# Performance work log

Hardware: AMD Instinct MI355X
Metric: run time of the kernel (lower is better)

## Reference

```python
import jax, jax.numpy as jnp
import numpy as np

B, T, N, D = 4, 8, 256, 1024
DH, KD, VD, IM, KC, H, L = 768, 576, 1152, 2048, 4, 12, 5
DK, DV = KD // H, VD // H

def _rms(x, w, eps=1e-6):
    return x * jax.lax.rsqrt(jnp.mean(x * x, -1, keepdims=True) + eps) * w

def _l2(x, eps=1e-6):
    return x * jax.lax.rsqrt(jnp.sum(x * x, -1, keepdims=True) + eps)

def _conv_silu(x, w):
    # depthwise causal conv1d over tokens: x [b,n,C], w [C,K]
    K = w.shape[1]
    xp = jnp.pad(x, ((0, 0), (K - 1, 0), (0, 0)))
    y = sum(xp[:, j:j + x.shape[1], :] * w[:, j] for j in range(K))
    return jax.nn.silu(y)

def _gdn_attn(x, p):
    b, n, _ = x.shape
    q = _l2(_conv_silu(x @ p['wq'].T, p['cq']).reshape(b, n, H, DK))
    k = _l2(_conv_silu(x @ p['wk'].T, p['ck']).reshape(b, n, H, DK))
    v = _conv_silu(x @ p['wv'].T, p['cv']).reshape(b, n, H, DV)
    beta = jax.nn.sigmoid(x @ p['wb'].T)                                   # [b,n,H]
    g = -jnp.exp(p['A_log']) * jax.nn.softplus(x @ p['wa'].T + p['dt_bias'])  # mamba-style log-decay
    scale = DK ** -0.5

    def step(S, inp):
        qt, kt, vt, gt, bt = inp
        S = S * jnp.exp(gt)[..., None, None]                               # [b,H,dk,dv] gated decay
        v_old = jnp.einsum('bhk,bhkv->bhv', kt, S)
        dv = bt[..., None] * (vt - v_old)                                  # delta rule update
        S = S + kt[..., None] * dv[:, :, None, :]
        o = jnp.einsum('bhk,bhkv->bhv', qt, S)
        return S, o

    xs = (jnp.moveaxis(q * scale, 1, 0), jnp.moveaxis(k, 1, 0), jnp.moveaxis(v, 1, 0),
          jnp.moveaxis(g, 1, 0), jnp.moveaxis(beta, 1, 0))
    S0 = jnp.zeros((b, H, DK, DV), x.dtype)
    _, o = jax.lax.scan(step, S0, xs)
    o = jnp.moveaxis(o, 0, 1)                                              # [b,n,H,dv]
    gate = (x @ p['wg'].T).reshape(b, n, H, DV)
    o = _rms(o, p['onorm']) * gate * jax.nn.sigmoid(gate)                  # RMSNorm + swish gate
    return o.reshape(b, n, VD) @ p['wo'].T

def _block(x, p):
    x = x + _gdn_attn(_rms(x, p['n1']), p)
    h = _rms(x, p['n2'])
    return x + (jax.nn.silu(h @ p['w1'].T) * (h @ p['w3'].T)) @ p['w2'].T

def _forward(z, actions, enc_w, enc_b, ap_w, ap_b, temb, ln_w, ln_b, dec_w, dec_b, lp, block_fn):
    zt = z.reshape(B, T, N, D)
    feat = zt @ enc_w.T + enc_b                                            # 1x1 conv == per-token linear
    act = jnp.broadcast_to(actions[:, :, None, :], (B, T, N, actions.shape[-1]))
    tok = jnp.concatenate([feat, act], -1) @ ap_w.T + ap_b
    tpos = jnp.minimum(jnp.arange(T), temb.shape[0] - 1)
    tok = tok + temb[tpos][None, :, None, :]
    x = tok.reshape(B * T, N, DH)                                          # timesteps independent -> fold into batch
    for i in range(L):
        p = {k: v[i] for k, v in lp.items()}
        x = block_fn(x, p)
    mu = jnp.mean(x, -1, keepdims=True)
    var = jnp.mean((x - mu) ** 2, -1, keepdims=True)
    x = (x - mu) * jax.lax.rsqrt(var + 1e-5) * ln_w + ln_b                 # final LayerNorm
    delta = x @ dec_w.T + dec_b
    return (zt + delta.reshape(B, T, N, D)).reshape(B, T * N, D)

def setup_inputs():
    key = jax.random.key(0)
    cnt = [0]
    def nrm(shape, s=0.02):
        cnt[0] += 1
        return jax.random.normal(jax.random.fold_in(key, cnt[0]), shape, jnp.float32) * s
    A = 2
    return dict(
        z=nrm((B, T * N, D), 1.0), actions=nrm((B, T, A), 1.0),
        enc_w=nrm((DH, D)), enc_b=jnp.zeros((DH,), jnp.float32),
        ap_w=nrm((DH, DH + A)), ap_b=jnp.zeros((DH,), jnp.float32),
        temb=nrm((T + 1, DH)),
        ln_w=jnp.ones((DH,), jnp.float32), ln_b=jnp.zeros((DH,), jnp.float32),
        dec_w=nrm((D, DH)), dec_b=jnp.zeros((D,), jnp.float32),
        n1=jnp.ones((L, DH), jnp.float32), n2=jnp.ones((L, DH), jnp.float32),
        wq=nrm((L, KD, DH)), cq=nrm((L, KD, KC), 0.3),
        wk=nrm((L, KD, DH)), ck=nrm((L, KD, KC), 0.3),
        wv=nrm((L, VD, DH)), cv=nrm((L, VD, KC), 0.3),
        wb=nrm((L, H, DH)), wa=nrm((L, H, DH)),
        A_log=jnp.log(jax.random.uniform(jax.random.fold_in(key, 777), (L, H), jnp.float32, 1.0, 16.0)),
        dt_bias=nrm((L, H), 0.1),
        wg=nrm((L, VD, DH)), onorm=jnp.ones((L, DV), jnp.float32),
        wo=nrm((L, DH, VD)),
        w1=nrm((L, IM, DH)), w2=nrm((L, DH, IM)), w3=nrm((L, IM, DH)),
    )

def reference(z, actions, enc_w, enc_b, ap_w, ap_b, temb, ln_w, ln_b, dec_w, dec_b,
              n1, n2, wq, cq, wk, ck, wv, cv, wb, wa, A_log, dt_bias, wg, onorm, wo, w1, w2, w3):
    lp = dict(n1=n1, n2=n2, wq=wq, cq=cq, wk=wk, ck=ck, wv=wv, cv=cv, wb=wb, wa=wa,
              A_log=A_log, dt_bias=dt_bias, wg=wg, onorm=onorm, wo=wo, w1=w1, w2=w2, w3=w3)
    return _forward(z, actions, enc_w, enc_b, ap_w, ap_b, temb, ln_w, ln_b, dec_w, dec_b, lp, _block)
```

## Files before the change

### kernel.cpp

```cpp
#include <hip/hip_runtime.h>
#include <math.h>

#define RTOT 8192
#define SEQL 256
#define DHC 768
#define KDC 576
#define VDC 1152
#define IMC 2048
#define NHC 12
#define DKC 48
#define DVC 96
#define NLAY 5

typedef float f4 __attribute__((ext_vector_type(4)));
typedef __bf16 v8bf __attribute__((ext_vector_type(8)));

__device__ __forceinline__ float sigmoidf_(float x){ return 1.0f/(1.0f+expf(-x)); }
__device__ __forceinline__ float siluf_(float x){ return x/(1.0f+expf(-x)); }

__device__ __forceinline__ void gl16(const void* g, void* l) {
    __builtin_amdgcn_global_load_lds((const __attribute__((address_space(1))) void*)g,
                                     (__attribute__((address_space(3))) void*)l, 16, 0, 0);
}
#define MFMA_BF16(a,b,c) __builtin_amdgcn_mfma_f32_16x16x32_bf16((a),(b),(c),0,0,0)

template<bool HASAL>
__global__ __launch_bounds__(256)
void gemm3_kernel(const __bf16* __restrict__ Ah, const __bf16* __restrict__ Al,
                  const __bf16* __restrict__ Wh, const __bf16* __restrict__ Wl,
                  int K, int ldc, int mode,
                  float* Cf, const float* bias, const float* bias2, const float* res,
                  __bf16* Ch, __bf16* Cl, const float* aux)
{
    __shared__ __bf16 sAh[128*32], sBh[128*32], sBl[128*32];
    __shared__ __bf16 sAl[HASAL ? 128*32 : 16];
    const int tid  = threadIdx.x;
    const int m0   = blockIdx.y * 128, n0 = blockIdx.x * 128;
    const int lane = tid & 63, wv = tid >> 6;
    const int wm   = (wv & 1) * 64, wn = (wv >> 1) * 64;

    const int o0 = tid * 16, o1 = o0 + 4096;
    const int r0 = o0 >> 6, s0 = (o0 >> 4) & 3;
    const int r1 = o1 >> 6, s1 = (o1 >> 4) & 3;
    const int k0 = (s0 ^ ((r0 >> 1) & 3)) * 8;
    const int k1 = (s1 ^ ((r1 >> 1) & 3)) * 8;

    const __bf16* gA0h = Ah + (size_t)(m0 + r0) * K + k0;
    const __bf16* gA1h = Ah + (size_t)(m0 + r1) * K + k1;
    const __bf16* gA0l = HASAL ? (Al + (size_t)(m0 + r0) * K + k0) : nullptr;
    const __bf16* gA1l = HASAL ? (Al + (size_t)(m0 + r1) * K + k1) : nullptr;
    const __bf16* gB0h = Wh + (size_t)(n0 + r0) * K + k0;
    const __bf16* gB1h = Wh + (size_t)(n0 + r1) * K + k1;
    const __bf16* gB0l = Wl + (size_t)(n0 + r0) * K + k0;
    const __bf16* gB1l = Wl + (size_t)(n0 + r1) * K + k1;

    const int fr = lane & 15, g8 = lane >> 4;
    int aoff[4], boff[4];
    #pragma unroll
    for (int f = 0; f < 4; ++f) {
        int ra = wm + f*16 + fr;
        aoff[f] = ra*32 + (g8 ^ ((ra >> 1) & 3)) * 8;
        int rb = wn + f*16 + fr;
        boff[f] = rb*32 + (g8 ^ ((rb >> 1) & 3)) * 8;
    }

    f4 acc[4][4];
    const f4 zero4 = {0.f, 0.f, 0.f, 0.f};
    #pragma unroll
    for (int i = 0; i < 4; ++i)
        #pragma unroll
        for (int j = 0; j < 4; ++j) acc[i][j] = zero4;

    for (int kt = 0; kt < K; kt += 32) {
        gl16(gA0h + kt, (char*)sAh + o0);
        gl16(gA1h + kt, (char*)sAh + o1);
        if constexpr (HASAL) {
            gl16(gA0l + kt, (char*)sAl + o0);
            gl16(gA1l + kt, (char*)sAl + o1);
        }
        gl16(gB0h + kt, (char*)sBh + o0);
        gl16(gB1h + kt, (char*)sBh + o1);
        gl16(gB0l + kt, (char*)sBl + o0);
        gl16(gB1l + kt, (char*)sBl + o1);
        __syncthreads();

        v8bf bhv[4], blv[4];
        #pragma unroll
        for (int f = 0; f < 4; ++f) {
            bhv[f] = *(const v8bf*)(sBh + boff[f]);
            blv[f] = *(const v8bf*)(sBl + boff[f]);
        }
        #pragma unroll
        for (int i = 0; i < 4; ++i) {
            v8bf ahv = *(const v8bf*)(sAh + aoff[i]);
            v8bf alv;
            if constexpr (HASAL) alv = *(const v8bf*)(sAl + aoff[i]);
            #pragma unroll
            for (int j = 0; j < 4; ++j) {
                f4 t = acc[i][j];
                if constexpr (HASAL) t = MFMA_BF16(alv, bhv[j], t);
                t = MFMA_BF16(ahv, blv[j], t);
                acc[i][j] = MFMA_BF16(ahv, bhv[j], t);
            }
        }
        __syncthreads();
    }

    const int rb4 = (lane >> 4) * 4;
    #pragma unroll
    for (int i = 0; i < 4; ++i) {
        #pragma unroll
        for (int jf = 0; jf < 4; ++jf) {
            int col = n0 + wn + jf*16 + fr;
            #pragma unroll
            for (int j = 0; j < 4; ++j) {
                int row = m0 + wm + i*16 + rb4 + j;
                size_t idx = (size_t)row * ldc + col;
                float v = acc[i][jf][j];
                if (bias)  v += bias[col];
                if (bias2) v += bias2[(size_t)(row >> 8) * ldc + col];
                if (res)   v += res[idx];
                if (mode == 2) v = siluf_(aux[idx]) * v;
                if (mode == 0) {
                    Cf[idx] = v;
                } else {
                    __bf16 h = (__bf16)v;
                    Ch[idx] = h;
                    if (Cl) Cl[idx] = (__bf16)(v - (float)h);
                }
            }
        }
    }
}

struct CvtBatch8 {
    const float* src[8];
    __bf16* dh[8];
    __bf16* dl[8];
    int ldv[8];
    int cols[8];
    int rowend[8];
};

__global__ __launch_bounds__(256)
void cvt_batch_kernel(CvtBatch8 b, int njobs)
{
    int r = blockIdx.x;
    int j = 0;
    while (j < njobs - 1 && r >= b.rowend[j]) ++j;
    int row0 = (j == 0) ? 0 : b.rowend[j-1];
    int lr = r - row0;
    const float* s = b.src[j] + (size_t)lr * b.ldv[j];
    __bf16* ph = b.dh[j] + (size_t)lr * b.cols[j];
    __bf16* pl = b.dl[j] + (size_t)lr * b.cols[j];
    int cols = b.cols[j];
    for (int c = threadIdx.x; c < cols; c += 256) {
        float v = s[c];
        __bf16 hh = (__bf16)v;
        ph[c] = hh;
        pl[c] = (__bf16)(v - (float)hh);
    }
}

__global__ __launch_bounds__(256)
void bias2_kernel(const float* __restrict__ actions, const float* __restrict__ ap_w,
                  const float* __restrict__ ap_b, const float* __restrict__ temb,
                  float* __restrict__ B2)
{
    int bt = blockIdx.x;
    int t  = bt & 7;
    float a0 = actions[bt*2], a1 = actions[bt*2+1];
    for (int c = threadIdx.x; c < DHC; c += 256)
        B2[bt*DHC + c] = ap_b[c] + temb[t*DHC + c] + a0*ap_w[c*770 + 768] + a1*ap_w[c*770 + 769];
}

__global__ __launch_bounds__(256)
void rmsnorm_kernel(const float* __restrict__ X, const float* __restrict__ w,
                    __bf16* __restrict__ Yh, __bf16* __restrict__ Yl)
{
    int row = blockIdx.x, tid = threadIdx.x;
    const float* xr = X + (size_t)row*DHC;
    float v0 = xr[tid], v1 = xr[tid+256], v2 = xr[tid+512];
    __shared__ float red[256];
    red[tid] = v0*v0 + v1*v1 + v2*v2;
    __syncthreads();
    for (int s = 128; s; s >>= 1) { if (tid < s) red[tid] += red[tid+s]; __syncthreads(); }
    float r = 1.0f/sqrtf(red[0]/768.0f + 1e-6f);
    float y0 = v0*r*w[tid], y1 = v1*r*w[tid+256], y2 = v2*r*w[tid+512];
    __bf16* ph = Yh + (size_t)row*DHC;
    __bf16* pl = Yl + (size_t)row*DHC;
    __bf16 h0 = (__bf16)y0, h1 = (__bf16)y1, h2 = (__bf16)y2;
    ph[tid] = h0;     pl[tid]     = (__bf16)(y0 - (float)h0);
    ph[tid+256] = h1; pl[tid+256] = (__bf16)(y1 - (float)h1);
    ph[tid+512] = h2; pl[tid+512] = (__bf16)(y2 - (float)h2);
}

__global__ __launch_bounds__(256)
void layernorm_kernel(const float* __restrict__ X, const float* __restrict__ w,
                      const float* __restrict__ b, __bf16* __restrict__ Yh,
                      __bf16* __restrict__ Yl)
{
    int row = blockIdx.x, tid = threadIdx.x;
    const float* xr = X + (size_t)row*DHC;
    float v0 = xr[tid], v1 = xr[tid+256], v2 = xr[tid+512];
    __shared__ float rs[256], rs2[256];
    rs[tid]  = v0+v1+v2;
    rs2[tid] = v0*v0+v1*v1+v2*v2;
    __syncthreads();
    for (int s = 128; s; s >>= 1) { if (tid < s) { rs[tid]+=rs[tid+s]; rs2[tid]+=rs2[tid+s]; } __syncthreads(); }
    float mu  = rs[0]/768.0f;
    float var = rs2[0]/768.0f - mu*mu;
    float r = 1.0f/sqrtf(var + 1e-5f);
    float y0 = (v0-mu)*r*w[tid]     + b[tid];
    float y1 = (v1-mu)*r*w[tid+256] + b[tid+256];
    float y2 = (v2-mu)*r*w[tid+512] + b[tid+512];
    __bf16* ph = Yh + (size_t)row*DHC;
    __bf16* pl = Yl + (size_t)row*DHC;
    __bf16 h0 = (__bf16)y0, h1 = (__bf16)y1, h2 = (__bf16)y2;
    ph[tid] = h0;     pl[tid]     = (__bf16)(y0 - (float)h0);
    ph[tid+256] = h1; pl[tid+256] = (__bf16)(y1 - (float)h1);
    ph[tid+512] = h2; pl[tid+512] = (__bf16)(y2 - (float)h2);
}

__global__ __launch_bounds__(64)
void convsilu_kernel(const float* __restrict__ P, int ldp, const float* __restrict__ cw,
                     float* __restrict__ Y, int ldd, int C)
{
    int c = blockIdx.x*64 + threadIdx.x;
    if (c >= C) return;
    int r = blockIdx.y;
    int t = r & (SEQL-1);
    float acc = P[(size_t)r*ldp + c] * cw[c*4+3];
    if (t >= 1) acc += P[(size_t)(r-1)*ldp + c] * cw[c*4+2];
    if (t >= 2) acc += P[(size_t)(r-2)*ldp + c] * cw[c*4+1];
    if (t >= 3) acc += P[(size_t)(r-3)*ldp + c] * cw[c*4+0];
    Y[(size_t)r*ldd + c] = siluf_(acc);
}

__global__ __launch_bounds__(128)
void l2norm_kernel(float* __restrict__ X, int ld, int col0, float scale)
{
    int row = blockIdx.x;
    int wave = threadIdx.x >> 6, lane = threadIdx.x & 63;
    #pragma unroll
    for (int i = 0; i < 6; ++i) {
        int h = wave*6 + i;
        size_t base = (size_t)row*ld + col0 + h*DKC;
        float v = (lane < DKC) ? X[base + lane] : 0.f;
        float ss = v*v;
        for (int off = 32; off; off >>= 1) ss += __shfl_down(ss, off);
        ss = __shfl(ss, 0);
        float r = scale / sqrtf(ss + 1e-6f);
        if (lane < DKC) X[base + lane] = v*r;
    }
}

__global__ __launch_bounds__(256)
void betag_kernel(const __bf16* __restrict__ XNh, const __bf16* __restrict__ XNl,
                  const float* __restrict__ wb, const float* __restrict__ wa,
                  const float* __restrict__ Alog, const float* __restrict__ dtb,
                  float* __restrict__ Beta, float* __restrict__ Dec)
{
    int row = blockIdx.x, tid = threadIdx.x;
    __shared__ float sx[DHC];
    for (int i = tid; i < DHC; i += 256)
        sx[i] = (float)XNh[(size_t)row*DHC + i] + (float)XNl[(size_t)row*DHC + i];
    __syncthreads();
    int wave = tid >> 6, lane = tid & 63;
    for (int d = 0; d < 6; ++d) {
        int out = wave*6 + d;
        const float* wr = (out < NHC) ? (wb + out*DHC) : (wa + (out-NHC)*DHC);
        float acc = 0.f;
        for (int j = lane; j < DHC; j += 64) acc += sx[j]*wr[j];
        for (int off = 32; off; off >>= 1) acc += __shfl_down(acc, off);
        if (lane == 0) {
            if (out < NHC) {
                Beta[(size_t)row*NHC + out] = sigmoidf_(acc);
            } else {
                int h = out - NHC;
                float sp = acc + dtb[h];
                sp = (sp > 20.f) ? sp : log1pf(expf(sp));
                Dec[(size_t)row*NHC + h] = expf(-expf(Alog[h]) * sp);
            }
        }
    }
}

#define SCAN_STEP_W(CUR, T)                                                  \
    {                                                                        \
        float dec  = sbuf[CUR][192], beta = sbuf[CUR][193];                  \
        const float* sk = &sbuf[CUR][0];                                     \
        const float* sq = &sbuf[CUR][48];                                    \
        const float* sv = &sbuf[CUR][96];                                    \
        float kx[12], qx[12], vx[6], pv[6], po[6];                           \
        _Pragma("unroll")                                                    \
        for (int i = 0; i < 12; ++i) { kx[i] = sk[rg*12+i]; qx[i] = sq[rg*12+i]; } \
        _Pragma("unroll")                                                    \
        for (int j = 0; j < 6; ++j) vx[j] = sv[g*6+j];                       \
        _Pragma("unroll")                                                    \
        for (int j = 0; j < 6; ++j) {                                        \
            float a0 = 0.f, a1 = 0.f;                                        \
            _Pragma("unroll")                                                \
            for (int i = 0; i < 12; i += 2) {                                \
                S[i][j]   *= dec; a0 += kx[i]  *S[i][j];                     \
                S[i+1][j] *= dec; a1 += kx[i+1]*S[i+1][j];                   \
            }                                                                \
            pv[j] = a0 + a1;                                                 \
        }                                                                    \
        _Pragma("unroll")                                                    \
        for (int j = 0; j < 6; ++j) {                                        \
            pv[j] += __shfl_xor(pv[j], 1);                                   \
            pv[j] += __shfl_xor(pv[j], 2);                                   \
        }                                                                    \
        _Pragma("unroll")                                                    \
        for (int j = 0; j < 6; ++j) {                                        \
            float dvv = beta * (vx[j] - pv[j]);                              \
            float a0 = 0.f, a1 = 0.f;                                        \
            _Pragma("unroll")                                                \
            for (int i = 0; i < 12; i += 2) {                                \
                S[i][j]   += kx[i]  *dvv; a0 += qx[i]  *S[i][j];             \
                S[i+1][j] += kx[i+1]*dvv; a1 += qx[i+1]*S[i+1][j];           \
            }                                                                \
            po[j] = a0 + a1;                                                 \
        }                                                                    \
        _Pragma("unroll")                                                    \
        for (int j = 0; j < 6; ++j) {                                        \
            po[j] += __shfl_xor(po[j], 1);                                   \
            po[j] += __shfl_xor(po[j], 2);                                   \
        }                                                                    \
        if (rg == 0) {                                                       \
            _Pragma("unroll")                                                \
            for (int j = 0; j < 6; ++j) op[(size_t)(T)*VDC + g*6 + j] = po[j]; \
        }                                                                    \
    }

__global__ __launch_bounds__(64)
void scan_kernel(const float* __restrict__ QKV, const float* __restrict__ Beta,
                 const float* __restrict__ Dec, float* __restrict__ O)
{
    int bid = blockIdx.x;
    int seq = bid / NHC, h = bid % NHC;
    int lane = threadIdx.x;
    int g = lane >> 2, rg = lane & 3;
    __shared__ float sbuf[2][194];

    float S[12][6];
    #pragma unroll
    for (int i = 0; i < 12; ++i)
        #pragma unroll
        for (int j = 0; j < 6; ++j) S[i][j] = 0.f;

    float* op = O + (size_t)seq*SEQL*VDC + h*DVC;

    const float* gp[4]; int gs[4]; bool en[4];
    #pragma unroll
    for (int s = 0; s < 4; ++s) {
        int e = lane + s*64;
        en[s] = (e < 194);
        const float* base = QKV;  int stride = 0;
        if (e < 48)        { base = QKV + (size_t)seq*SEQL*2304 + 576 + h*DKC + e;          stride = 2304; }
        else if (e < 96)   { base = QKV + (size_t)seq*SEQL*2304 + h*DKC + (e-48);           stride = 2304; }
        else if (e < 192)  { base = QKV + (size_t)seq*SEQL*2304 + 1152 + h*DVC + (e-96);    stride = 2304; }
        else if (e == 192) { base = Dec  + (size_t)seq*SEQL*NHC + h;                        stride = NHC; }
        else if (e == 193) { base = Beta + (size_t)seq*SEQL*NHC + h;                        stride = NHC; }
        gp[s] = base; gs[s] = stride;
    }

    float pA[4], pB[4];
    #pragma unroll
    for (int s = 0; s < 4; ++s)
        if (en[s]) { sbuf[0][lane + s*64] = gp[s][0]; pA[s] = gp[s][gs[s]]; }
    __syncthreads();

    int cur = 0;
    for (int t = 0; t < SEQL; t += 2) {
        {
            int tn = t + 2; if (tn > SEQL-1) tn = SEQL-1;
            #pragma unroll
            for (int s = 0; s < 4; ++s) if (en[s]) pB[s] = gp[s][(size_t)tn * gs[s]];
            SCAN_STEP_W(cur, t)
            #pragma unroll
            for (int s = 0; s < 4; ++s) if (en[s]) sbuf[cur^1][lane + s*64] = pA[s];
            __syncthreads();
            cur ^= 1;
        }
        {
            int tn = t + 3; if (tn > SEQL-1) tn = SEQL-1;
            #pragma unroll
            for (int s = 0; s < 4; ++s) if (en[s]) pA[s] = gp[s][(size_t)tn * gs[s]];
            SCAN_STEP_W(cur, t+1)
            #pragma unroll
            for (int s = 0; s < 4; ++s) if (en[s]) sbuf[cur^1][lane + s*64] = pB[s];
            __syncthreads();
            cur ^= 1;
        }
    }
}

__global__ __launch_bounds__(128)
void opost_kernel(const float* __restrict__ O, const float* __restrict__ G, int ldg,
                  const float* __restrict__ onorm, __bf16* __restrict__ Oh,
                  __bf16* __restrict__ Ol)
{
    int row = blockIdx.x;
    int wave = threadIdx.x >> 6, lane = threadIdx.x & 63;
    #pragma unroll
    for (int i = 0; i < 6; ++i) {
        int h = wave*6 + i;
        size_t baseO = (size_t)row*VDC + h*DVC;
        size_t baseG = (size_t)row*ldg + h*DVC;
        float a = O[baseO + lane];
        float c = (lane < 32) ? O[baseO + 64 + lane] : 0.f;
        float ss = a*a + c*c;
        for (int off = 32; off; off >>= 1) ss += __shfl_down(ss, off);
        ss = __shfl(ss, 0);
        float r = 1.0f/sqrtf(ss/96.0f + 1e-6f);
        float ga = G[baseG + lane];
        float v0 = a*r*onorm[lane]*ga*sigmoidf_(ga);
        { __bf16 hh = (__bf16)v0; Oh[baseO+lane] = hh; Ol[baseO+lane] = (__bf16)(v0 - (float)hh); }
        if (lane < 32) {
            float gb = G[baseG + 64 + lane];
            float v1 = c*r*onorm[64+lane]*gb*sigmoidf_(gb);
            __bf16 hh = (__bf16)v1; Oh[baseO+64+lane] = hh; Ol[baseO+64+lane] = (__bf16)(v1 - (float)hh);
        }
    }
}

static inline void gemm3(bool hasAl,
                         const __bf16* Ah, const __bf16* Al, const __bf16* Wh, const __bf16* Wl,
                         int K, int ldc, int mode, float* Cf, const float* bias,
                         const float* bias2, const float* res, __bf16* Ch, __bf16* Cl,
                         const float* aux, hipStream_t s)
{
    dim3 grid(ldc/128, RTOT/128);
    if (hasAl)
        hipLaunchKernelGGL(gemm3_kernel<true>,  grid, dim3(256), 0, s, Ah, Al, Wh, Wl, K, ldc, mode,
                           Cf, bias, bias2, res, Ch, Cl, aux);
    else
        hipLaunchKernelGGL(gemm3_kernel<false>, grid, dim3(256), 0, s, Ah, Al, Wh, Wl, K, ldc, mode,
                           Cf, bias, bias2, res, Ch, Cl, aux);
}

extern "C" void kernel_launch(void* const* d_in, const int* in_sizes, int n_in,
                              void* d_out, int out_size, void* d_ws, size_t ws_size,
                              hipStream_t stream)
{
    const float* z       = (const float*)d_in[0];
    const float* actions = (const float*)d_in[1];
    const float* enc_w   = (const float*)d_in[2];
    const float* enc_b   = (const float*)d_in[3];
    const float* ap_w    = (const float*)d_in[4];
    const float* ap_b    = (const float*)d_in[5];
    const float* temb    = (const float*)d_in[6];
    const float* ln_w    = (const float*)d_in[7];
    const float* ln_b    = (const float*)d_in[8];
    const float* dec_w   = (const float*)d_in[9];
    const float* dec_b   = (const float*)d_in[10];
    const float* n1      = (const float*)d_in[11];
    const float* n2      = (const float*)d_in[12];
    const float* wq      = (const float*)d_in[13];
    const float* cq      = (const float*)d_in[14];
    const float* wk      = (const float*)d_in[15];
    const float* ck      = (const float*)d_in[16];
    const float* wv      = (const float*)d_in[17];
    const float* cv      = (const float*)d_in[18];
    const float* wb      = (const float*)d_in[19];
    const float* wa      = (const float*)d_in[20];
    const float* A_log   = (const float*)d_in[21];
    const float* dt_bias = (const float*)d_in[22];
    const float* wg      = (const float*)d_in[23];
    const float* onorm   = (const float*)d_in[24];
    const float* wo      = (const float*)d_in[25];
    const float* w1      = (const float*)d_in[26];
    const float* w2      = (const float*)d_in[27];
    const float* w3      = (const float*)d_in[28];

    const size_t R = RTOT;
    const float qscale = 0.14433756729740643f;

    float* X    = (float*)d_ws;
    float* BUF1 = X    + 768*R;
    float* O    = BUF1 + 1152*R;
    float* QKV  = O    + 1152*R;
    float* BETA = QKV  + 2304*R;
    float* DEC  = BETA + 12*R;
    float* TMP  = DEC  + 12*R;
    __bf16* XNh = (__bf16*)(TMP + 32*768);
    __bf16* XNl = XNh + 768*R;
    __bf16* WS0 = XNl + 768*R;

    const size_t need = (size_t)(768+1152+1152+2304+24)*R*4 + 32*768*4
                      + ((size_t)1536*R + 16515072)*2;
    if (ws_size < need) return;

    __bf16* zh  = (__bf16*)QKV;
    __bf16* zl  = zh + 1024*R;
    __bf16* Oh  = (__bf16*)QKV;
    __bf16* Ol  = Oh + 1152*R;
    float*  A1f = QKV;
    __bf16* A1h = (__bf16*)BUF1;

    {
        __bf16* ench = WS0;                       __bf16* encl = ench + (size_t)768*1024;
        __bf16* aph  = encl + (size_t)768*1024;   __bf16* apl  = aph  + (size_t)768*768;

        CvtBatch8 eb{};
        eb.src[0]=z;     eb.dh[0]=zh;   eb.dl[0]=zl;   eb.ldv[0]=1024; eb.cols[0]=1024; eb.rowend[0]=8192;
        eb.src[1]=enc_w; eb.dh[1]=ench; eb.dl[1]=encl; eb.ldv[1]=1024; eb.cols[1]=1024; eb.rowend[1]=8960;
        eb.src[2]=ap_w;  eb.dh[2]=aph;  eb.dl[2]=apl;  eb.ldv[2]=770;  eb.cols[2]=768;  eb.rowend[2]=9728;
        hipLaunchKernelGGL(cvt_batch_kernel, dim3(9728), dim3(256), 0, stream, eb, 3);

        hipLaunchKernelGGL(bias2_kernel, dim3(32), dim3(256), 0, stream, actions, ap_w, ap_b, temb, TMP);
        gemm3(true, zh, zl, ench, encl, 1024, 768, 1, nullptr, enc_b, nullptr, nullptr, XNh, XNl, nullptr, stream);
        gemm3(true, XNh, XNl, aph, apl, 768, 768, 0, X, nullptr, TMP, nullptr, nullptr, nullptr, nullptr, stream);
    }

    for (int l = 0; l < NLAY; ++l) {
        __bf16* qkh = WS0;                        __bf16* qkl = qkh + (size_t)1152*768;
        __bf16* vh  = qkl + (size_t)1152*768;     __bf16* vl  = vh  + (size_t)1152*768;
        __bf16* gh  = vl  + (size_t)1152*768;     __bf16* gl_ = gh  + (size_t)1152*768;
        __bf16* woh = gl_ + (size_t)1152*768;     __bf16* wol = woh + (size_t)768*1152;
        __bf16* w1h = wol + (size_t)768*1152;     __bf16* w1l = w1h + (size_t)2048*768;
        __bf16* w3h = w1l + (size_t)2048*768;     __bf16* w3l = w3h + (size_t)2048*768;
        __bf16* w2h = w3l + (size_t)2048*768;     __bf16* w2l = w2h + (size_t)768*2048;

        CvtBatch8 lb{};
        lb.src[0]=wq + (size_t)l*KDC*DHC; lb.dh[0]=qkh;                   lb.dl[0]=qkl;                   lb.ldv[0]=768;  lb.cols[0]=768;  lb.rowend[0]=576;
        lb.src[1]=wk + (size_t)l*KDC*DHC; lb.dh[1]=qkh+(size_t)576*768;   lb.dl[1]=qkl+(size_t)576*768;   lb.ldv[1]=768;  lb.cols[1]=768;  lb.rowend[1]=1152;
        lb.src[2]=wv + (size_t)l*VDC*DHC; lb.dh[2]=vh;                    lb.dl[2]=vl;                    lb.ldv[2]=768;  lb.cols[2]=768;  lb.rowend[2]=2304;
        lb.src[3]=wg + (size_t)l*VDC*DHC; lb.dh[3]=gh;                    lb.dl[3]=gl_;                   lb.ldv[3]=768;  lb.cols[3]=768;  lb.rowend[3]=3456;
        lb.src[4]=wo + (size_t)l*DHC*VDC; lb.dh[4]=woh;                   lb.dl[4]=wol;                   lb.ldv[4]=1152; lb.cols[4]=1152; lb.rowend[4]=4224;
        lb.src[5]=w1 + (size_t)l*IMC*DHC; lb.dh[5]=w1h;                   lb.dl[5]=w1l;                   lb.ldv[5]=768;  lb.cols[5]=768;  lb.rowend[5]=6272;
        lb.src[6]=w3 + (size_t)l*IMC*DHC; lb.dh[6]=w3h;                   lb.dl[6]=w3l;                   lb.ldv[6]=768;  lb.cols[6]=768;  lb.rowend[6]=8320;
        lb.src[7]=w2 + (size_t)l*DHC*IMC; lb.dh[7]=w2h;                   lb.dl[7]=w2l;                   lb.ldv[7]=2048; lb.cols[7]=2048; lb.rowend[7]=9088;
        hipLaunchKernelGGL(cvt_batch_kernel, dim3(9088), dim3(256), 0, stream, lb, 8);

        hipLaunchKernelGGL(rmsnorm_kernel, dim3(RTOT), dim3(256), 0, stream, X, n1 + l*DHC, XNh, XNl);

        gemm3(false, XNh, nullptr, qkh, qkl, 768, 1152, 0, BUF1, nullptr, nullptr, nullptr, nullptr, nullptr, nullptr, stream);
        hipLaunchKernelGGL(convsilu_kernel, dim3(9,  RTOT), dim3(64), 0, stream, BUF1,       1152, cq + (size_t)l*KDC*4, QKV,        2304, KDC);
        hipLaunchKernelGGL(convsilu_kernel, dim3(9,  RTOT), dim3(64), 0, stream, BUF1 + 576, 1152, ck + (size_t)l*KDC*4, QKV + 576,  2304, KDC);
        gemm3(false, XNh, nullptr, vh, vl, 768, 1152, 0, BUF1, nullptr, nullptr, nullptr, nullptr, nullptr, nullptr, stream);
        hipLaunchKernelGGL(convsilu_kernel, dim3(18, RTOT), dim3(64), 0, stream, BUF1,       1152, cv + (size_t)l*VDC*4, QKV + 1152, 2304, VDC);
        gemm3(false, XNh, nullptr, gh, gl_, 768, 1152, 0, BUF1, nullptr, nullptr, nullptr, nullptr, nullptr, nullptr, stream);
        hipLaunchKernelGGL(betag_kernel, dim3(RTOT), dim3(256), 0, stream,
                           XNh, XNl, wb + (size_t)l*NHC*DHC, wa + (size_t)l*NHC*DHC,
                           A_log + l*NHC, dt_bias + l*NHC, BETA, DEC);

        hipLaunchKernelGGL(l2norm_kernel, dim3(RTOT), dim3(128), 0, stream, QKV, 2304, 0,   qscale);
        hipLaunchKernelGGL(l2norm_kernel, dim3(RTOT), dim3(128), 0, stream, QKV, 2304, 576, 1.0f);

        hipLaunchKernelGGL(scan_kernel, dim3(32*NHC), dim3(64), 0, stream, QKV, BETA, DEC, O);

        hipLaunchKernelGGL(opost_kernel, dim3(RTOT), dim3(128), 0, stream, O, BUF1, 1152,
                           onorm + l*DVC, Oh, Ol);
        gemm3(true, Oh, Ol, woh, wol, 1152, 768, 0, X, nullptr, nullptr, X, nullptr, nullptr, nullptr, stream);

        hipLaunchKernelGGL(rmsnorm_kernel, dim3(RTOT), dim3(256), 0, stream, X, n2 + l*DHC, XNh, XNl);
        gemm3(false, XNh, nullptr, w1h, w1l, 768, 2048, 0, A1f, nullptr, nullptr, nullptr, nullptr, nullptr, nullptr, stream);
        gemm3(false, XNh, nullptr, w3h, w3l, 768, 2048, 2, nullptr, nullptr, nullptr, nullptr, A1h, nullptr, A1f, stream);
        gemm3(false, A1h, nullptr, w2h, w2l, 2048, 768, 0, X, nullptr, nullptr, X, nullptr, nullptr, nullptr, stream);
    }

    {
        __bf16* dech = WS0;  __bf16* decl = dech + (size_t)1024*768;
        CvtBatch8 db{};
        db.src[0]=dec_w; db.dh[0]=dech; db.dl[0]=decl; db.ldv[0]=768; db.cols[0]=768; db.rowend[0]=1024;
        hipLaunchKernelGGL(cvt_batch_kernel, dim3(1024), dim3(256), 0, stream, db, 1);
        hipLaunchKernelGGL(layernorm_kernel, dim3(RTOT), dim3(256), 0, stream, X, ln_w, ln_b, XNh, XNl);
        gemm3(true, XNh, XNl, dech, decl, 768, 1024, 0, (float*)d_out, dec_b, nullptr, z, nullptr, nullptr, nullptr, stream);
    }
}
```

Measured before the change: 5.796 ms.

## Split scan state across six blocks per head and drop LDS staging

The delta-rule scan kernel now launches six blocks per (sequence, head). Each block owns 16 of the 96 value columns, so every thread holds a 12-element state column instead of a 12x6 tile. The shared-memory double buffer and its per-step barriers are replaced by direct register prefetch of four tokens ahead with vectorized float4 loads. This aims to raise occupancy from 384 latency-bound blocks and to shorten the per-step dependency chain, at the cost of each block redundantly loading k, q, decay and beta.

```diff
diff --git a/kernel.cpp b/kernel.cpp
--- a/kernel.cpp
+++ b/kernel.cpp
@@ -286,114 +286,87 @@
     }
 }
 
-#define SCAN_STEP_W(CUR, T)                                                  \
-    {                                                                        \
-        float dec  = sbuf[CUR][192], beta = sbuf[CUR][193];                  \
-        const float* sk = &sbuf[CUR][0];                                     \
-        const float* sq = &sbuf[CUR][48];                                    \
-        const float* sv = &sbuf[CUR][96];                                    \
-        float kx[12], qx[12], vx[6], pv[6], po[6];                           \
-        _Pragma("unroll")                                                    \
-        for (int i = 0; i < 12; ++i) { kx[i] = sk[rg*12+i]; qx[i] = sq[rg*12+i]; } \
-        _Pragma("unroll")                                                    \
-        for (int j = 0; j < 6; ++j) vx[j] = sv[g*6+j];                       \
-        _Pragma("unroll")                                                    \
-        for (int j = 0; j < 6; ++j) {                                        \
-            float a0 = 0.f, a1 = 0.f;                                        \
-            _Pragma("unroll")                                                \
-            for (int i = 0; i < 12; i += 2) {                                \
-                S[i][j]   *= dec; a0 += kx[i]  *S[i][j];                     \
-                S[i+1][j] *= dec; a1 += kx[i+1]*S[i+1][j];                   \
-            }                                                                \
-            pv[j] = a0 + a1;                                                 \
-        }                                                                    \
-        _Pragma("unroll")                                                    \
-        for (int j = 0; j < 6; ++j) {                                        \
-            pv[j] += __shfl_xor(pv[j], 1);                                   \
-            pv[j] += __shfl_xor(pv[j], 2);                                   \
-        }                                                                    \
-        _Pragma("unroll")                                                    \
-        for (int j = 0; j < 6; ++j) {                                        \
-            float dvv = beta * (vx[j] - pv[j]);                              \
-            float a0 = 0.f, a1 = 0.f;                                        \
-            _Pragma("unroll")                                                \
-            for (int i = 0; i < 12; i += 2) {                                \
-                S[i][j]   += kx[i]  *dvv; a0 += qx[i]  *S[i][j];             \
-                S[i+1][j] += kx[i+1]*dvv; a1 += qx[i+1]*S[i+1][j];           \
-            }                                                                \
-            po[j] = a0 + a1;                                                 \
-        }                                                                    \
-        _Pragma("unroll")                                                    \
-        for (int j = 0; j < 6; ++j) {                                        \
-            po[j] += __shfl_xor(po[j], 1);                                   \
-            po[j] += __shfl_xor(po[j], 2);                                   \
-        }                                                                    \
-        if (rg == 0) {                                                       \
-            _Pragma("unroll")                                                \
-            for (int j = 0; j < 6; ++j) op[(size_t)(T)*VDC + g*6 + j] = po[j]; \
-        }                                                                    \
-    }
+struct Tok { float k[12]; float q[12]; float v, d, b; };
+
+__device__ __forceinline__ void tok_load(Tok& T, const float* kp, const float* qp,
+                                         const float* vp, const float* dp,
+                                         const float* bp, int t)
+{
+    size_t ro = (size_t)t * 2304;
+    *(float4*)&T.k[0] = *(const float4*)(kp + ro);
+    *(float4*)&T.k[4] = *(const float4*)(kp + ro + 4);
+    *(float4*)&T.k[8] = *(const float4*)(kp + ro + 8);
+    *(float4*)&T.q[0] = *(const float4*)(qp + ro);
+    *(float4*)&T.q[4] = *(const float4*)(qp + ro + 4);
+    *(float4*)&T.q[8] = *(const float4*)(qp + ro + 8);
+    T.v = vp[ro];
+    T.d = dp[(size_t)t * NHC];
+    T.b = bp[(size_t)t * NHC];
+}
+
+__device__ __forceinline__ void scan_step(const Tok& Tk, float S[12], int rg,
+                                          float* op, int T)
+{
+    float dec = Tk.d, beta = Tk.b;
+    float pv0 = 0.f, pv1 = 0.f;
+    #pragma unroll
+    for (int i = 0; i < 12; i += 2) {
+        S[i]   *= dec; pv0 += Tk.k[i]  * S[i];
+        S[i+1] *= dec; pv1 += Tk.k[i+1]* S[i+1];
+    }
+    float pv = pv0 + pv1;
+    pv += __shfl_xor(pv, 1); pv += __shfl_xor(pv, 2);
+    float dvv = beta * (Tk.v - pv);
+    float po0 = 0.f, po1 = 0.f;
+    #pragma unroll
+    for (int i = 0; i < 12; i += 2) {
+        S[i]   += Tk.k[i]  * dvv; po0 += Tk.q[i]  * S[i];
+        S[i+1] += Tk.k[i+1]* dvv; po1 += Tk.q[i+1]* S[i+1];
+    }
+    float po = po0 + po1;
+    po += __shfl_xor(po, 1); po += __shfl_xor(po, 2);
+    if (rg == 0) op[(size_t)T * VDC] = po;
+}
 
 __global__ __launch_bounds__(64)
 void scan_kernel(const float* __restrict__ QKV, const float* __restrict__ Beta,
                  const float* __restrict__ Dec, float* __restrict__ O)
 {
-    int bid = blockIdx.x;
-    int seq = bid / NHC, h = bid % NHC;
+    int bid   = blockIdx.x;
+    int chunk = bid % 6;
+    int sh    = bid / 6;
+    int seq = sh / NHC, h = sh % NHC;
     int lane = threadIdx.x;
-    int g = lane >> 2, rg = lane & 3;
-    __shared__ float sbuf[2][194];
-
-    float S[12][6];
-    #pragma unroll
-    for (int i = 0; i < 12; ++i)
-        #pragma unroll
-        for (int j = 0; j < 6; ++j) S[i][j] = 0.f;
-
-    float* op = O + (size_t)seq*SEQL*VDC + h*DVC;
-
-    const float* gp[4]; int gs[4]; bool en[4];
-    #pragma unroll
-    for (int s = 0; s < 4; ++s) {
-        int e = lane + s*64;
-        en[s] = (e < 194);
-        const float* base = QKV;  int stride = 0;
-        if (e < 48)        { base = QKV + (size_t)seq*SEQL*2304 + 576 + h*DKC + e;          stride = 2304; }
-        else if (e < 96)   { base = QKV + (size_t)seq*SEQL*2304 + h*DKC + (e-48);           stride = 2304; }
-        else if (e < 192)  { base = QKV + (size_t)seq*SEQL*2304 + 1152 + h*DVC + (e-96);    stride = 2304; }
-        else if (e == 192) { base = Dec  + (size_t)seq*SEQL*NHC + h;                        stride = NHC; }
-        else if (e == 193) { base = Beta + (size_t)seq*SEQL*NHC + h;                        stride = NHC; }
-        gp[s] = base; gs[s] = stride;
-    }
-
-    float pA[4], pB[4];
-    #pragma unroll
-    for (int s = 0; s < 4; ++s)
-        if (en[s]) { sbuf[0][lane + s*64] = gp[s][0]; pA[s] = gp[s][gs[s]]; }
-    __syncthreads();
-
-    int cur = 0;
-    for (int t = 0; t < SEQL; t += 2) {
-        {
-            int tn = t + 2; if (tn > SEQL-1) tn = SEQL-1;
-            #pragma unroll
-            for (int s = 0; s < 4; ++s) if (en[s]) pB[s] = gp[s][(size_t)tn * gs[s]];
-            SCAN_STEP_W(cur, t)
-            #pragma unroll
-            for (int s = 0; s < 4; ++s) if (en[s]) sbuf[cur^1][lane + s*64] = pA[s];
-            __syncthreads();
-            cur ^= 1;
-        }
-        {
-            int tn = t + 3; if (tn > SEQL-1) tn = SEQL-1;
-            #pragma unroll
-            for (int s = 0; s < 4; ++s) if (en[s]) pA[s] = gp[s][(size_t)tn * gs[s]];
-            SCAN_STEP_W(cur, t+1)
-            #pragma unroll
-            for (int s = 0; s < 4; ++s) if (en[s]) sbuf[cur^1][lane + s*64] = pB[s];
-            __syncthreads();
-            cur ^= 1;
-        }
+    int col = chunk*16 + (lane >> 2);
+    int rg  = lane & 3;
+
+    const float* rowb = QKV + (size_t)seq*SEQL*2304;
+    const float* kp = rowb + 576  + h*DKC + rg*12;
+    const float* qp = rowb +        h*DKC + rg*12;
+    const float* vp = rowb + 1152 + h*DVC + col;
+    const float* dp = Dec  + (size_t)seq*SEQL*NHC + h;
+    const float* bp = Beta + (size_t)seq*SEQL*NHC + h;
+    float* op = O + (size_t)seq*SEQL*VDC + h*DVC + col;
+
+    float S[12];
+    #pragma unroll
+    for (int i = 0; i < 12; ++i) S[i] = 0.f;
+
+    Tok A, B, C, D;
+    tok_load(A, kp, qp, vp, dp, bp, 0);
+    tok_load(B, kp, qp, vp, dp, bp, 1);
+    tok_load(C, kp, qp, vp, dp, bp, 2);
+    tok_load(D, kp, qp, vp, dp, bp, 3);
+
+    for (int t = 0; t < SEQL; t += 4) {
+        scan_step(A, S, rg, op, t);
+        if (t + 4 < SEQL) tok_load(A, kp, qp, vp, dp, bp, t + 4);
+        scan_step(B, S, rg, op, t + 1);
+        if (t + 5 < SEQL) tok_load(B, kp, qp, vp, dp, bp, t + 5);
+        scan_step(C, S, rg, op, t + 2);
+        if (t + 6 < SEQL) tok_load(C, kp, qp, vp, dp, bp, t + 6);
+        scan_step(D, S, rg, op, t + 3);
+        if (t + 7 < SEQL) tok_load(D, kp, qp, vp, dp, bp, t + 7);
     }
 }
 
@@ -550,7 +523,7 @@
         hipLaunchKernelGGL(l2norm_kernel, dim3(RTOT), dim3(128), 0, stream, QKV, 2304, 0,   qscale);
         hipLaunchKernelGGL(l2norm_kernel, dim3(RTOT), dim3(128), 0, stream, QKV, 2304, 576, 1.0f);
 
-        hipLaunchKernelGGL(scan_kernel, dim3(32*NHC), dim3(64), 0, stream, QKV, BETA, DEC, O);
+        hipLaunchKernelGGL(scan_kernel, dim3(32*NHC*6), dim3(64), 0, stream, QKV, BETA, DEC, O);
 
         hipLaunchKernelGGL(opost_kernel, dim3(RTOT), dim3(128), 0, stream, O, BUF1, 1152,
                            onorm + l*DVC, Oh, Ol);
```

Result: faster. 5.321 ms (-8.2%).
